# Kernel tuning notes

Measured on AMD Instinct MI355X. Metric: run time of the kernel, lower is better.

Reference implementation:

```python
import jax, jax.numpy as jnp
import numpy as np

B = 4096
IND = 512
OUTD = 512
DEG = 2
P = 2  # dim_treat
KNOTS = [[0.33, 0.66], [0.33, 0.66]]
D = DEG + 1 + len(KNOTS[0])  # 5 basis functions per treatment dim


def setup_inputs() -> dict:
    key = jax.random.key(0)
    k1, k2, k3 = jax.random.split(key, 3)
    x = jax.random.uniform(k1, (B, P + IND), dtype=jnp.float32)  # treat dims in [0,1]
    weight = jax.random.uniform(k2, (IND, OUTD, D ** P), dtype=jnp.float32)  # torch.rand init
    bias = jax.random.uniform(k3, (OUTD, D ** P), dtype=jnp.float32)
    return {"x": x, "weight": weight, "bias": bias}


def _truncated_power_basis(x_treat):
    # x_treat: [B, P] -> basis: [B, P, D]
    knots = jnp.asarray(KNOTS, dtype=x_treat.dtype)  # [P, n_knots]
    # polynomial part: 1, x, x^2, ... x^DEG
    pows = jnp.stack([x_treat ** i for i in range(DEG + 1)], axis=-1)  # [B, P, DEG+1]
    # truncated part: relu(x - knot)^DEG  (DEG > 1 branch of original code)
    trunc = jax.nn.relu(x_treat[:, :, None] - knots[None, :, :]) ** DEG  # [B, P, n_knots]
    return jnp.concatenate([pows, trunc], axis=-1)


def reference(x, weight, bias):
    x_treat = x[:, :P]          # [B, P]
    x_feature = x[:, P:]        # [B, IND]
    basis = _truncated_power_basis(x_treat)  # [B, P, D]
    # Kronecker product across the two treatment dims: outer product, flattened
    kb = jnp.einsum('bi,bj->bij', basis[:, 0, :], basis[:, 1, :]).reshape(x.shape[0], D * P * 0 + D * D)  # [B, D^2]
    # fused: (weight^T @ x_feature) contracted with the per-sample basis coefficients
    out = jnp.einsum('bi,iod,bd->bo', x_feature, weight, kb)  # [B, OUTD]
    out = out + kb @ bias.T      # bias also varies with treatment basis
    out = jax.nn.relu(out)       # act='relu'
    # islastlayer=0: re-attach treatment dims
    return jnp.concatenate([x_treat, out], axis=1)  # [B, P + OUTD]
```

## Files before the change

### kernel.cpp

```cpp
#include <hip/hip_runtime.h>
#include <hip/hip_bf16.h>
#include <string.h>

#define NB    4096
#define IND_  512
#define OUTD_ 512
#define XCOLS 514
#define ND    25
#define KTOT  12800
#define KT2B  12928
#define NSPL  4

#define BM 128
#define BN 128
#define BKB 128

#define PWI 64
#define PWO 4
#define PWC (PWO * ND)
#define T8P 112

typedef float  f32x4  __attribute__((ext_vector_type(4)));
typedef int    i32x4  __attribute__((ext_vector_type(4)));
typedef int    i32x8  __attribute__((ext_vector_type(8)));
typedef unsigned short u16x4 __attribute__((ext_vector_type(4)));
typedef unsigned int   u32x2 __attribute__((ext_vector_type(2)));

__device__ __forceinline__ unsigned short f2bf(float f) {
  unsigned int x = __float_as_uint(f);
  return (unsigned short)((x + 0x7fffu + ((x >> 16) & 1u)) >> 16);
}

__device__ __forceinline__ float bf2f(unsigned short u) {
  return __uint_as_float(((unsigned int)u) << 16);
}

__device__ __forceinline__ unsigned int pk_bf16(float a, float b) {
  return (unsigned int)f2bf(a) | ((unsigned int)f2bf(b) << 16);
}

__device__ __forceinline__ unsigned char f2fp8(float v) {
  if (v < 0.015625f) {
    return (unsigned char)__float2int_rn(v * 512.0f);
  }
  unsigned int u = __float_as_uint(v);
  u += 0x7ffffu + ((u >> 20) & 1u);
  int e = (int)(u >> 23) - 127 + 7;
  unsigned int m = (u >> 20) & 7u;
  return (unsigned char)((e << 3) | m);
}

__device__ __forceinline__ float basis_f(float t, int j) {
  switch (j) {
    case 0: return 1.0f;
    case 1: return t;
    case 2: return t * t;
    case 3: { float r = t - 0.33f; r = r > 0.0f ? r : 0.0f; return r * r; }
    default:{ float r = t - 0.66f; r = r > 0.0f ? r : 0.0f; return r * r; }
  }
}

__device__ __forceinline__ void gload_lds16(const void* g, void* l) {
  __builtin_amdgcn_global_load_lds(
      (const __attribute__((address_space(1))) void*)g,
      (__attribute__((address_space(3))) void*)l, 16, 0, 0);
}

__global__ __launch_bounds__(256) void prep_all_kernel(
    const float* __restrict__ x, const float* __restrict__ W,
    const float* __restrict__ bias, unsigned char* __restrict__ Xf8,
    float* __restrict__ kb, unsigned char* __restrict__ kbT8,
    unsigned char* __restrict__ Wf8, float* __restrict__ out)
{
  __shared__ unsigned char tile8[PWI * T8P];
  const int bid = blockIdx.x;
  const int tid = threadIdx.x;

  if (bid < 512) {
    const int lane = tid & 63;
    #pragma unroll
    for (int rr = 0; rr < 2; ++rr) {
      const int b = bid * 8 + (tid >> 6) * 2 + rr;
      const float* xr = x + (size_t)b * XCOLS;
      const float* fp = xr + 2 + lane * 8;
      float2 a0 = *(const float2*)(fp + 0);
      float2 a1 = *(const float2*)(fp + 2);
      float2 a2 = *(const float2*)(fp + 4);
      float2 a3 = *(const float2*)(fp + 6);
      float xf[8] = {a0.x, a0.y, a1.x, a1.y, a2.x, a2.y, a3.x, a3.y};
      u32x2 pk;
      pk[0] = (unsigned int)f2fp8(xf[0]) | ((unsigned int)f2fp8(xf[1]) << 8) |
              ((unsigned int)f2fp8(xf[2]) << 16) | ((unsigned int)f2fp8(xf[3]) << 24);
      pk[1] = (unsigned int)f2fp8(xf[4]) | ((unsigned int)f2fp8(xf[5]) << 8) |
              ((unsigned int)f2fp8(xf[6]) << 16) | ((unsigned int)f2fp8(xf[7]) << 24);
      *reinterpret_cast<u32x2*>(Xf8 + (size_t)b * IND_ + lane * 8) = pk;

      float t0 = xr[0], t1 = xr[1];
      if (lane < 2) out[(size_t)b * XCOLS + lane] = (lane == 0) ? t0 : t1;
      {
        int d1 = lane / 5, d2 = lane - d1 * 5;
        float kv = basis_f(t0, d1) * basis_f(t1, d2);
        if (lane < ND) kb[(size_t)b * ND + lane] = kv;
      }
      {
        int ta = 2 * lane, tb = 2 * lane + 1;
        unsigned char ba = 0, bb = 0;
        if (ta < ND) { int d1 = ta / 5, d2 = ta - d1 * 5;
                       ba = f2fp8(basis_f(t0, d1) * basis_f(t1, d2)); }
        if (tb < ND) { int d1 = tb / 5, d2 = tb - d1 * 5;
                       bb = f2fp8(basis_f(t0, d1) * basis_f(t1, d2)); }
        *(unsigned short*)(kbT8 + (size_t)b * 128 + 2 * lane) =
            (unsigned short)ba | ((unsigned short)bb << 8);
      }
    }
  } else {
    const int pw = bid - 512;
    const int i0 = (pw & 7) * PWI;
    const int o0 = (pw >> 3) * PWO;

    for (int t = tid; t < PWI * (PWC / 4); t += 256) {
      int il = t / (PWC / 4);
      int c4 = t - il * (PWC / 4);
      float4 v = *(const float4*)(W + ((size_t)(i0 + il) * OUTD_ + o0) * ND + c4 * 4);
      unsigned int pk = (unsigned int)f2fp8(v.x) | ((unsigned int)f2fp8(v.y) << 8) |
                        ((unsigned int)f2fp8(v.z) << 16) | ((unsigned int)f2fp8(v.w) << 24);
      *(unsigned int*)&tile8[il * T8P + c4 * 4] = pk;
    }
    __syncthreads();

    for (int g = tid; g < PWC * (PWI / 8); g += 256) {
      int c  = g >> 3;
      int ig = g & 7;
      int d  = c % 25;
      int o_l = c / 25;
      unsigned long long v = 0;
      #pragma unroll
      for (int jj = 0; jj < 8; ++jj)
        v |= (unsigned long long)tile8[(ig * 8 + jj) * T8P + c] << (8 * jj);
      size_t rowb = (size_t)(o0 + o_l) * KT2B + (size_t)d * IND_ + i0;
      *reinterpret_cast<unsigned long long*>(Wf8 + rowb + ig * 8) = v;
    }

    if ((pw & 7) == 0) {
      int o = o0 + (tid >> 6);
      int p = tid & 63;
      int ta = 2 * p, tb = 2 * p + 1;
      unsigned char ba = (ta < ND) ? f2fp8(bias[o * ND + ta]) : (unsigned char)0;
      unsigned char bb = (tb < ND) ? f2fp8(bias[o * ND + tb]) : (unsigned char)0;
      *(unsigned short*)(Wf8 + (size_t)o * KT2B + KTOT + 2 * p) =
          (unsigned short)ba | ((unsigned short)bb << 8);
    }
  }
}

__global__ __launch_bounds__(256, 2) void gemm_mx_kernel(
    const unsigned char* __restrict__ Wf8, const unsigned char* __restrict__ Xf8,
    const float* __restrict__ kb, const unsigned char* __restrict__ kbT8,
    unsigned short* __restrict__ Pb)
{
  __shared__ unsigned char Als[BM * BKB];
  __shared__ unsigned char Bls[BN * BKB];

  const int tid  = threadIdx.x;
  const int lane = tid & 63;
  const int w    = tid >> 6;
  const int l15  = lane & 15;
  const int quad = lane >> 4;

  const int id  = blockIdx.x;
  const int xcd = id & 7;
  const int j   = id >> 3;
  const int bx  = j & 3;
  const int pg  = xcd * 16 + (j >> 2);
  const int by  = pg & 31;
  const int bz  = pg >> 5;

  const int o0 = bx * BM;
  const int b0 = by * BN;
  const int ks_begin = bz * 3200;
  const int ks_end   = (bz == 3) ? KT2B : ks_begin + 3200;

  const int o_off = (w & 1) * 64;
  const int b_off = (w >> 1) * 64;
  const int srow  = lane >> 3;
  const int scol  = ((lane & 7) ^ srow) * 16;
  const int r7    = l15 & 7;
  const int s0    = ((2 * quad) ^ r7) * 16;
  const int s1    = ((2 * quad + 1) ^ r7) * 16;

  f32x4 acc[4][4], fin[4][4];
  #pragma unroll
  for (int i = 0; i < 4; ++i)
    #pragma unroll
    for (int jj = 0; jj < 4; ++jj) { acc[i][jj] = (f32x4)0.0f; fin[i][jj] = (f32x4)0.0f; }

  float kv[4] = {1.0f, 1.0f, 1.0f, 1.0f};
  int cur_d = -1;

  for (int k0 = ks_begin; k0 < ks_end; k0 += BKB) {
    const int d = k0 >> 9;
    if (d != cur_d) {
      if (cur_d >= 0) {
        #pragma unroll
        for (int nf = 0; nf < 4; ++nf)
          #pragma unroll
          for (int mf = 0; mf < 4; ++mf)
            #pragma unroll
            for (int r = 0; r < 4; ++r) {
              fin[mf][nf][r] += kv[nf] * acc[mf][nf][r];
              acc[mf][nf][r] = 0.0f;
            }
      }
      cur_d = d;
      if (d < ND) {
        #pragma unroll
        for (int nf = 0; nf < 4; ++nf)
          kv[nf] = kb[(size_t)(b0 + b_off + nf * 16 + l15) * ND + d];
      } else {
        #pragma unroll
        for (int nf = 0; nf < 4; ++nf) kv[nf] = 1.0f;
      }
    }

    #pragma unroll
    for (int c = 0; c < 4; ++c) {
      int chunk = w * 4 + c;
      int r = chunk * 8 + srow;
      gload_lds16(Wf8 + (size_t)(o0 + r) * KT2B + k0 + scol, &Als[chunk * 1024]);
      const unsigned char* gb = (d < ND)
          ? Xf8 + (size_t)(b0 + r) * IND_ + (k0 & 511) + scol
          : kbT8 + (size_t)(b0 + r) * 128 + scol;
      gload_lds16(gb, &Bls[chunk * 1024]);
    }
    __syncthreads();

    {
      i32x8 af[4], bfr[4];
      #pragma unroll
      for (int mf = 0; mf < 4; ++mf) {
        int rb = (o_off + mf * 16 + l15) * BKB;
        i32x4 lo = *reinterpret_cast<const i32x4*>(&Als[rb + s0]);
        i32x4 hi = *reinterpret_cast<const i32x4*>(&Als[rb + s1]);
        i32x8 v;
        v[0] = lo[0]; v[1] = lo[1]; v[2] = lo[2]; v[3] = lo[3];
        v[4] = hi[0]; v[5] = hi[1]; v[6] = hi[2]; v[7] = hi[3];
        af[mf] = v;
      }
      #pragma unroll
      for (int nf = 0; nf < 4; ++nf) {
        int rb = (b_off + nf * 16 + l15) * BKB;
        i32x4 lo = *reinterpret_cast<const i32x4*>(&Bls[rb + s0]);
        i32x4 hi = *reinterpret_cast<const i32x4*>(&Bls[rb + s1]);
        i32x8 v;
        v[0] = lo[0]; v[1] = lo[1]; v[2] = lo[2]; v[3] = lo[3];
        v[4] = hi[0]; v[5] = hi[1]; v[6] = hi[2]; v[7] = hi[3];
        bfr[nf] = v;
      }
      #pragma unroll
      for (int mf = 0; mf < 4; ++mf)
        #pragma unroll
        for (int nf = 0; nf < 4; ++nf)
          acc[mf][nf] = __builtin_amdgcn_mfma_scale_f32_16x16x128_f8f6f4(
              af[mf], bfr[nf], acc[mf][nf],
              0, 0, 0, 0x7f7f7f7f, 0, 0x7f7f7f7f);
    }
    __syncthreads();
  }

  #pragma unroll
  for (int nf = 0; nf < 4; ++nf)
    #pragma unroll
    for (int mf = 0; mf < 4; ++mf)
      #pragma unroll
      for (int r = 0; r < 4; ++r)
        fin[mf][nf][r] += kv[nf] * acc[mf][nf][r];

  unsigned short* Pz = Pb + (size_t)bz * NB * OUTD_;
  #pragma unroll
  for (int mf = 0; mf < 4; ++mf)
    #pragma unroll
    for (int nf = 0; nf < 4; ++nf) {
      int bg = b0 + b_off + nf * 16 + l15;
      int og = o0 + o_off + mf * 16 + quad * 4;
      u32x2 pk;
      pk[0] = pk_bf16(fin[mf][nf][0], fin[mf][nf][1]);
      pk[1] = pk_bf16(fin[mf][nf][2], fin[mf][nf][3]);
      *reinterpret_cast<u32x2*>(&Pz[(size_t)bg * OUTD_ + og]) = pk;
    }
}

__global__ __launch_bounds__(256) void epilogue_kernel(
    const unsigned short* __restrict__ Pb, float* __restrict__ out)
{
  const int idx = (blockIdx.x * 256 + threadIdx.x) * 4;
  const int b = idx >> 9;
  const int o = idx & 511;
  const size_t ps = (size_t)NB * OUTD_;
  float s[4] = {0.0f, 0.0f, 0.0f, 0.0f};
  #pragma unroll
  for (int z = 0; z < NSPL; ++z) {
    u16x4 v = *reinterpret_cast<const u16x4*>(&Pb[z * ps + idx]);
    #pragma unroll
    for (int e = 0; e < 4; ++e) s[e] += bf2f(v[e]);
  }
  float* op = out + (size_t)b * XCOLS + 2 + o;
  float2 lo, hi;
  lo.x = s[0] > 0.0f ? s[0] : 0.0f;
  lo.y = s[1] > 0.0f ? s[1] : 0.0f;
  hi.x = s[2] > 0.0f ? s[2] : 0.0f;
  hi.y = s[3] > 0.0f ? s[3] : 0.0f;
  *(float2*)op = lo;
  *(float2*)(op + 2) = hi;
}

extern "C" void kernel_launch(void* const* d_in, const int* in_sizes, int n_in,
                              void* d_out, int out_size, void* d_ws, size_t ws_size,
                              hipStream_t stream) {
  const float* x    = (const float*)d_in[0];
  const float* W    = (const float*)d_in[1];
  const float* bias = (const float*)d_in[2];
  float* out = (float*)d_out;
  char* ws = (char*)d_ws;

  const size_t xf_off  = 0;
  const size_t wf_off  = 2097152;
  const size_t kb_off  = wf_off + (size_t)OUTD_ * KT2B;
  const size_t kbt_off = kb_off + 409600;
  const size_t p_off   = kbt_off + (size_t)NB * 128;
  unsigned char* Xf8  = (unsigned char*)(ws + xf_off);
  unsigned char* Wf8  = (unsigned char*)(ws + wf_off);
  float* kb           = (float*)(ws + kb_off);
  unsigned char* kbT8 = (unsigned char*)(ws + kbt_off);
  unsigned short* Pb  = (unsigned short*)(ws + p_off);

  prep_all_kernel<<<1536, 256, 0, stream>>>(x, W, bias, Xf8, kb, kbT8, Wf8, out);
  gemm_mx_kernel<<<512, 256, 0, stream>>>(Wf8, Xf8, kb, kbT8, Pb);
  epilogue_kernel<<<(NB * OUTD_) / 1024, 256, 0, stream>>>(Pb, out);
}
```

Baseline: 127.3 us.

## Double-buffer LDS tiles to overlap global loads with MFMA compute

Splits the A and B shared-memory tiles into two buffers and prefetches the next K tile with direct global-to-LDS loads while the current tile feeds the scaled FP8 MFMAs. Each iteration ends with an explicit full wait on memory counters and a barrier. This is meant to hide global load latency behind matrix work. It doubles LDS use to 64KB per block, which may cut occupancy under launch_bounds(256,2).

```diff
diff --git a/kernel.cpp b/kernel.cpp
--- a/kernel.cpp
+++ b/kernel.cpp
@@ -64,6 +64,10 @@
   __builtin_amdgcn_global_load_lds(
       (const __attribute__((address_space(1))) void*)g,
       (__attribute__((address_space(3))) void*)l, 16, 0, 0);
+}
+
+__device__ __forceinline__ void drain_all() {
+  asm volatile("s_waitcnt vmcnt(0) lgkmcnt(0)" ::: "memory");
 }
 
 __global__ __launch_bounds__(256) void prep_all_kernel(
@@ -158,8 +162,8 @@
     const float* __restrict__ kb, const unsigned char* __restrict__ kbT8,
     unsigned short* __restrict__ Pb)
 {
-  __shared__ unsigned char Als[BM * BKB];
-  __shared__ unsigned char Bls[BN * BKB];
+  __shared__ unsigned char Als[2][BM * BKB];
+  __shared__ unsigned char Bls[2][BN * BKB];
 
   const int tid  = threadIdx.x;
   const int lane = tid & 63;
@@ -179,6 +183,7 @@
   const int b0 = by * BN;
   const int ks_begin = bz * 3200;
   const int ks_end   = (bz == 3) ? KT2B : ks_begin + 3200;
+  const int nIter    = (ks_end - ks_begin) / BKB;
 
   const int o_off = (w & 1) * 64;
   const int b_off = (w >> 1) * 64;
@@ -197,7 +202,31 @@
   float kv[4] = {1.0f, 1.0f, 1.0f, 1.0f};
   int cur_d = -1;
 
-  for (int k0 = ks_begin; k0 < ks_end; k0 += BKB) {
+  auto issueAB = [&](int k0, int buf) {
+    const int dd = k0 >> 9;
+    #pragma unroll
+    for (int c = 0; c < 4; ++c) {
+      int chunk = w * 4 + c;
+      int r = chunk * 8 + srow;
+      gload_lds16(Wf8 + (size_t)(o0 + r) * KT2B + k0 + scol, &Als[buf][chunk * 1024]);
+      const unsigned char* gb = (dd < ND)
+          ? Xf8 + (size_t)(b0 + r) * IND_ + (k0 & 511) + scol
+          : kbT8 + (size_t)(b0 + r) * 128 + scol;
+      gload_lds16(gb, &Bls[buf][chunk * 1024]);
+    }
+  };
+
+  issueAB(ks_begin, 0);
+  drain_all();
+  __syncthreads();
+
+  for (int n = 0; n < nIter; ++n) {
+    const int k0 = ks_begin + n * BKB;
+    const int p  = n & 1;
+    const int q  = p ^ 1;
+
+    if (n + 1 < nIter) issueAB(k0 + BKB, q);
+
     const int d = k0 >> 9;
     if (d != cur_d) {
       if (cur_d >= 0) {
@@ -222,25 +251,13 @@
       }
     }
 
-    #pragma unroll
-    for (int c = 0; c < 4; ++c) {
-      int chunk = w * 4 + c;
-      int r = chunk * 8 + srow;
-      gload_lds16(Wf8 + (size_t)(o0 + r) * KT2B + k0 + scol, &Als[chunk * 1024]);
-      const unsigned char* gb = (d < ND)
-          ? Xf8 + (size_t)(b0 + r) * IND_ + (k0 & 511) + scol
-          : kbT8 + (size_t)(b0 + r) * 128 + scol;
-      gload_lds16(gb, &Bls[chunk * 1024]);
-    }
-    __syncthreads();
-
     {
       i32x8 af[4], bfr[4];
       #pragma unroll
       for (int mf = 0; mf < 4; ++mf) {
         int rb = (o_off + mf * 16 + l15) * BKB;
-        i32x4 lo = *reinterpret_cast<const i32x4*>(&Als[rb + s0]);
-        i32x4 hi = *reinterpret_cast<const i32x4*>(&Als[rb + s1]);
+        i32x4 lo = *reinterpret_cast<const i32x4*>(&Als[p][rb + s0]);
+        i32x4 hi = *reinterpret_cast<const i32x4*>(&Als[p][rb + s1]);
         i32x8 v;
         v[0] = lo[0]; v[1] = lo[1]; v[2] = lo[2]; v[3] = lo[3];
         v[4] = hi[0]; v[5] = hi[1]; v[6] = hi[2]; v[7] = hi[3];
@@ -249,8 +266,8 @@
       #pragma unroll
       for (int nf = 0; nf < 4; ++nf) {
         int rb = (b_off + nf * 16 + l15) * BKB;
-        i32x4 lo = *reinterpret_cast<const i32x4*>(&Bls[rb + s0]);
-        i32x4 hi = *reinterpret_cast<const i32x4*>(&Bls[rb + s1]);
+        i32x4 lo = *reinterpret_cast<const i32x4*>(&Bls[p][rb + s0]);
+        i32x4 hi = *reinterpret_cast<const i32x4*>(&Bls[p][rb + s1]);
         i32x8 v;
         v[0] = lo[0]; v[1] = lo[1]; v[2] = lo[2]; v[3] = lo[3];
         v[4] = hi[0]; v[5] = hi[1]; v[6] = hi[2]; v[7] = hi[3];
@@ -264,6 +281,8 @@
               af[mf], bfr[nf], acc[mf][nf],
               0, 0, 0, 0x7f7f7f7f, 0, 0x7f7f7f7f);
     }
+
+    drain_all();
     __syncthreads();
   }
 
```

After: 124.2 us. 2.4% less time.
